# Kernel tuning notes

Measured on AMD Instinct MI355X. Metric: run time of the kernel, lower is better.

The kernel has to match this reference:

```python
import jax, jax.numpy as jnp
import numpy as np

N = 50000      # nodes
E = 800000     # edges (avg degree 16)
D_IN = 128
H = 128
D_OUT = 32


def setup_inputs() -> dict:
    key = jax.random.key(0)
    ks = jax.random.split(key, 12)
    s = 0.05
    return {
        "x": jax.random.normal(ks[0], (N, D_IN), jnp.float32),
        "edge_index": jax.random.randint(ks[1], (2, E), 0, N, jnp.int32),
        "W_in": jax.random.normal(ks[2], (D_IN, H), jnp.float32) * s,
        "b_in": jnp.zeros((H,), jnp.float32),
        "W_msg0": jax.random.normal(ks[3], (H, H), jnp.float32) * s,
        "gru_wih0": jax.random.normal(ks[4], (3 * H, H), jnp.float32) * s,
        "gru_whh0": jax.random.normal(ks[5], (3 * H, H), jnp.float32) * s,
        "gru_bih0": jnp.zeros((3 * H,), jnp.float32),
        "gru_bhh0": jnp.zeros((3 * H,), jnp.float32),
        "W_msg1": jax.random.normal(ks[6], (H, H), jnp.float32) * s,
        "gru_wih1": jax.random.normal(ks[7], (3 * H, H), jnp.float32) * s,
        "gru_whh1": jax.random.normal(ks[8], (3 * H, H), jnp.float32) * s,
        "gru_bih1": jnp.zeros((3 * H,), jnp.float32),
        "gru_bhh1": jnp.zeros((3 * H,), jnp.float32),
        "W_out": jax.random.normal(ks[9], (H, D_OUT), jnp.float32) * s,
        "b_out": jnp.zeros((D_OUT,), jnp.float32),
    }


def _gated_layer(h, src, dst, W_msg, wih, whh, bih, bhh):
    # GatedGraphConv (num_layers=1): linear -> scatter-add over edges -> GRU update
    m = h @ W_msg                                           # [N, H]
    agg = jax.ops.segment_sum(m[src], dst, num_segments=N)  # gather at src, add at dst
    gi = agg @ wih.T + bih                                  # [N, 3H]
    gh = h @ whh.T + bhh                                    # [N, 3H]
    i_r, i_z, i_n = jnp.split(gi, 3, axis=-1)
    h_r, h_z, h_n = jnp.split(gh, 3, axis=-1)
    r = jax.nn.sigmoid(i_r + h_r)
    z = jax.nn.sigmoid(i_z + h_z)
    n = jnp.tanh(i_n + r * h_n)
    return (1.0 - z) * n + z * h


def reference(x, edge_index, W_in, b_in,
              W_msg0, gru_wih0, gru_whh0, gru_bih0, gru_bhh0,
              W_msg1, gru_wih1, gru_whh1, gru_bih1, gru_bhh1,
              W_out, b_out):
    src, dst = edge_index[0], edge_index[1]
    h = jax.nn.relu(x @ W_in + b_in)
    h = _gated_layer(h, src, dst, W_msg0, gru_wih0, gru_whh0, gru_bih0, gru_bhh0)
    h = _gated_layer(h, src, dst, W_msg1, gru_wih1, gru_whh1, gru_bih1, gru_bhh1)
    return h @ W_out + b_out
```

## Files before the change

### kernel.cpp

```cpp
#include <hip/hip_runtime.h>
#include <hip/hip_bf16.h>
#include <math.h>

#define NN 50000
#define NE 800000
#define HD 128
#define SCAN_BLOCKS 196
#define FILL_CHUNK 4096
#define FILL_CHUNKS ((NE + FILL_CHUNK - 1) / FILL_CHUNK)
#define NPART 8

typedef __attribute__((ext_vector_type(8))) short bf16x8;
typedef __attribute__((ext_vector_type(4))) float f32x4;

__device__ inline float b2f(unsigned short s) {
    union { unsigned int u; float f; } w; w.u = ((unsigned int)s) << 16; return w.f;
}
__device__ inline short f2b(float f) {
    __hip_bfloat16 h = __float2bfloat16(f);
    short s; __builtin_memcpy(&s, &h, 2); return s;
}

__global__ void hist_kernel(const int* __restrict__ dst, int* __restrict__ counts) {
    int e = blockIdx.x * blockDim.x + threadIdx.x;
    if (e < NE) atomicAdd(&counts[dst[e]], 1);
}

__global__ __launch_bounds__(256) void scan_partial_kernel(const int* __restrict__ counts,
                                                           int* __restrict__ partial) {
    __shared__ int sm[256];
    int i = blockIdx.x * 256 + threadIdx.x;
    sm[threadIdx.x] = (i < NN) ? counts[i] : 0;
    __syncthreads();
    for (int off = 128; off > 0; off >>= 1) {
        if (threadIdx.x < off) sm[threadIdx.x] += sm[threadIdx.x + off];
        __syncthreads();
    }
    if (threadIdx.x == 0) partial[blockIdx.x] = sm[0];
}

__global__ __launch_bounds__(256) void scan_base_kernel(const int* __restrict__ partial,
                                                        int* __restrict__ base) {
    __shared__ int sm[256];
    int tid = threadIdx.x;
    int v = (tid < SCAN_BLOCKS) ? partial[tid] : 0;
    sm[tid] = v;
    __syncthreads();
    for (int off = 1; off < 256; off <<= 1) {
        int t = (tid >= off) ? sm[tid - off] : 0;
        __syncthreads();
        sm[tid] += t;
        __syncthreads();
    }
    if (tid < SCAN_BLOCKS) base[tid] = sm[tid] - v;
}

__global__ __launch_bounds__(256) void scan_final_kernel(const int* __restrict__ counts,
                                                         const int* __restrict__ base,
                                                         int* __restrict__ offsets,
                                                         int* __restrict__ cursor) {
    __shared__ int sm[256];
    int tid = threadIdx.x;
    int i = blockIdx.x * 256 + tid;
    int v = (i < NN) ? counts[i] : 0;
    sm[tid] = v;
    __syncthreads();
    for (int off = 1; off < 256; off <<= 1) {
        int t = (tid >= off) ? sm[tid - off] : 0;
        __syncthreads();
        sm[tid] += t;
        __syncthreads();
    }
    if (i < NN) {
        int o = base[blockIdx.x] + sm[tid] - v;
        offsets[i] = o;
        cursor[i]  = o;
        if (i == NN - 1) offsets[NN] = o + v;
    }
}

__global__ __launch_bounds__(256) void fill_part_kernel(const int* __restrict__ src,
                                                        const int* __restrict__ dst,
                                                        int* __restrict__ cursor,
                                                        int* __restrict__ perm_src) {
    int part  = blockIdx.x & (NPART - 1);
    int chunk = blockIdx.x >> 3;
    int lo = part * (NN / NPART);
    int hi = (part == NPART - 1) ? NN : lo + (NN / NPART);
    int e0 = chunk * FILL_CHUNK;
    int e1 = min(e0 + FILL_CHUNK, NE);
    for (int e = e0 + threadIdx.x; e < e1; e += 256) {
        int d = dst[e];
        if (d >= lo && d < hi) {
            int pos = atomicAdd(&cursor[d], 1);
            perm_src[pos] = src[e];
        }
    }
}

__global__ void pack_all(const float* W_in, const float* W_msg0, const float* W_msg1,
                         const float* W_out, const float* wih0, const float* whh0,
                         const float* wih1, const float* whh1,
                         short* pWin, short* pWm0, short* pWm1, short* pWout,
                         short* pI0, short* pH0, short* pI1, short* pH1) {
    const float* src; short* dst; int JT; bool kmajor; int J;
    switch (blockIdx.y) {
        case 0: src = W_in;   dst = pWin;  JT = 8;  kmajor = true;  J = 128; break;
        case 1: src = W_msg0; dst = pWm0;  JT = 8;  kmajor = true;  J = 128; break;
        case 2: src = W_msg1; dst = pWm1;  JT = 8;  kmajor = true;  J = 128; break;
        case 3: src = W_out;  dst = pWout; JT = 2;  kmajor = true;  J = 32;  break;
        case 4: src = wih0;   dst = pI0;   JT = 24; kmajor = false; J = 384; break;
        case 5: src = whh0;   dst = pH0;   JT = 24; kmajor = false; J = 384; break;
        case 6: src = wih1;   dst = pI1;   JT = 24; kmajor = false; J = 384; break;
        default: src = whh1;  dst = pH1;   JT = 24; kmajor = false; J = 384; break;
    }
    int t = blockIdx.x * 256 + threadIdx.x;
    if (t >= JT * 4 * 64) return;
    int l = t & 63, ks = (t >> 6) & 3, jt = t >> 8;
    int j = jt * 16 + (l & 15);
    int k0 = ks * 32 + (l >> 4) * 8;
    bf16x8 tv;
    if (kmajor) {
        #pragma unroll
        for (int i = 0; i < 8; ++i) tv[i] = f2b(src[(k0 + i) * J + j]);
    } else {
        #pragma unroll
        for (int i = 0; i < 8; ++i) tv[i] = f2b(src[j * 128 + k0 + i]);
    }
    *reinterpret_cast<bf16x8*>(dst + t * 8) = tv;
}

template<int JT, bool RELU, bool AF32, bool OUTF32>
__global__ __launch_bounds__(256) void gemm_mfma(const void* __restrict__ Av,
                                                 const short* __restrict__ Bp,
                                                 const float* __restrict__ bias,
                                                 void* __restrict__ Cv) {
    int w = threadIdx.x >> 6;
    int l = threadIdx.x & 63;
    int r0 = blockIdx.x * 128 + w * 32;
    int lr = l & 15;
    int lk = (l >> 4) * 8;

    bf16x8 a[2][4];
    #pragma unroll
    for (int mt = 0; mt < 2; ++mt) {
        int row = r0 + mt * 16 + lr;
        if (row > NN - 1) row = NN - 1;
        #pragma unroll
        for (int ks = 0; ks < 4; ++ks) {
            if (AF32) {
                const float* ap = (const float*)Av + (size_t)row * HD + ks * 32 + lk;
                float4 v0 = *(const float4*)ap;
                float4 v1 = *(const float4*)(ap + 4);
                bf16x8 tv;
                tv[0] = f2b(v0.x); tv[1] = f2b(v0.y); tv[2] = f2b(v0.z); tv[3] = f2b(v0.w);
                tv[4] = f2b(v1.x); tv[5] = f2b(v1.y); tv[6] = f2b(v1.z); tv[7] = f2b(v1.w);
                a[mt][ks] = tv;
            } else {
                a[mt][ks] = *reinterpret_cast<const bf16x8*>((const short*)Av + (size_t)row * HD + ks * 32 + lk);
            }
        }
    }

    #pragma unroll
    for (int jt = 0; jt < JT; ++jt) {
        f32x4 acc0 = {0.f, 0.f, 0.f, 0.f}, acc1 = {0.f, 0.f, 0.f, 0.f};
        const short* bp = Bp + ((jt * 4) * 64 + l) * 8;
        #pragma unroll
        for (int ks = 0; ks < 4; ++ks) {
            bf16x8 b = *reinterpret_cast<const bf16x8*>(bp + ks * 64 * 8);
            acc0 = __builtin_amdgcn_mfma_f32_16x16x32_bf16(a[0][ks], b, acc0, 0, 0, 0);
            acc1 = __builtin_amdgcn_mfma_f32_16x16x32_bf16(a[1][ks], b, acc1, 0, 0, 0);
        }
        int col = jt * 16 + lr;
        float bs = bias ? bias[col] : 0.f;
        #pragma unroll
        for (int mt = 0; mt < 2; ++mt) {
            f32x4 acc = mt ? acc1 : acc0;
            #pragma unroll
            for (int rg = 0; rg < 4; ++rg) {
                int row = r0 + mt * 16 + (l >> 4) * 4 + rg;
                if (row < NN) {
                    float v = acc[rg] + bs;
                    if (RELU) v = fmaxf(v, 0.f);
                    if (OUTF32) ((float*)Cv)[(size_t)row * (16 * JT) + col] = v;
                    else        ((short*)Cv)[(size_t)row * (16 * JT) + col] = f2b(v);
                }
            }
        }
    }
}

__global__ __launch_bounds__(256) void aggregate_bf16(const short* __restrict__ m,
                                                      const int* __restrict__ offsets,
                                                      const int* __restrict__ perm_src,
                                                      short* __restrict__ agg) {
    int node = blockIdx.x * 8 + (threadIdx.x >> 5);
    if (node >= NN) return;
    int q = (threadIdx.x & 31) * 4;
    int beg = offsets[node], end = offsets[node + 1];
    float a0 = 0.f, a1 = 0.f, a2 = 0.f, a3 = 0.f;
    int e = beg;
    for (; e + 2 <= end; e += 2) {
        int s0 = perm_src[e], s1 = perm_src[e + 1];
        ushort4 u0 = *reinterpret_cast<const ushort4*>(m + (size_t)s0 * HD + q);
        ushort4 u1 = *reinterpret_cast<const ushort4*>(m + (size_t)s1 * HD + q);
        a0 += b2f(u0.x) + b2f(u1.x);
        a1 += b2f(u0.y) + b2f(u1.y);
        a2 += b2f(u0.z) + b2f(u1.z);
        a3 += b2f(u0.w) + b2f(u1.w);
    }
    if (e < end) {
        ushort4 u = *reinterpret_cast<const ushort4*>(m + (size_t)perm_src[e] * HD + q);
        a0 += b2f(u.x); a1 += b2f(u.y); a2 += b2f(u.z); a3 += b2f(u.w);
    }
    ushort4 o;
    o.x = (unsigned short)f2b(a0); o.y = (unsigned short)f2b(a1);
    o.z = (unsigned short)f2b(a2); o.w = (unsigned short)f2b(a3);
    *reinterpret_cast<ushort4*>(agg + (size_t)node * HD + q) = o;
}

__global__ __launch_bounds__(256) void gru_mfma(const short* __restrict__ agg,
                                                const short* __restrict__ h,
                                                const short* __restrict__ BpI,
                                                const short* __restrict__ BpH,
                                                const float* __restrict__ bih,
                                                const float* __restrict__ bhh,
                                                short* __restrict__ hout) {
    int w = threadIdx.x >> 6;
    int l = threadIdx.x & 63;
    int r0 = blockIdx.x * 64 + w * 16;
    int lr = l & 15;
    int lk = (l >> 4) * 8;

    bf16x8 aa[4], ah[4];
    {
        int row = r0 + lr;
        if (row > NN - 1) row = NN - 1;
        #pragma unroll
        for (int ks = 0; ks < 4; ++ks) {
            aa[ks] = *reinterpret_cast<const bf16x8*>(agg + (size_t)row * HD + ks * 32 + lk);
            ah[ks] = *reinterpret_cast<const bf16x8*>(h   + (size_t)row * HD + ks * 32 + lk);
        }
    }

    const f32x4 zero = {0.f, 0.f, 0.f, 0.f};
    #pragma unroll 1
    for (int jt = 0; jt < 8; ++jt) {
        f32x4 ir = zero, iz = zero, in_ = zero;
        f32x4 hr = zero, hz = zero, hn = zero;
        #pragma unroll
        for (int ks = 0; ks < 4; ++ks) {
            const short* bi = BpI + ((jt * 4 + ks) * 64 + l) * 8;
            const short* bh = BpH + ((jt * 4 + ks) * 64 + l) * 8;
            bf16x8 bir = *reinterpret_cast<const bf16x8*>(bi);
            bf16x8 biz = *reinterpret_cast<const bf16x8*>(bi + 8 * 4 * 64 * 8);
            bf16x8 bin = *reinterpret_cast<const bf16x8*>(bi + 16 * 4 * 64 * 8);
            bf16x8 bhr = *reinterpret_cast<const bf16x8*>(bh);
            bf16x8 bhz = *reinterpret_cast<const bf16x8*>(bh + 8 * 4 * 64 * 8);
            bf16x8 bhn = *reinterpret_cast<const bf16x8*>(bh + 16 * 4 * 64 * 8);
            ir  = __builtin_amdgcn_mfma_f32_16x16x32_bf16(aa[ks], bir, ir,  0, 0, 0);
            iz  = __builtin_amdgcn_mfma_f32_16x16x32_bf16(aa[ks], biz, iz,  0, 0, 0);
            in_ = __builtin_amdgcn_mfma_f32_16x16x32_bf16(aa[ks], bin, in_, 0, 0, 0);
            hr  = __builtin_amdgcn_mfma_f32_16x16x32_bf16(ah[ks], bhr, hr,  0, 0, 0);
            hz  = __builtin_amdgcn_mfma_f32_16x16x32_bf16(ah[ks], bhz, hz,  0, 0, 0);
            hn  = __builtin_amdgcn_mfma_f32_16x16x32_bf16(ah[ks], bhn, hn,  0, 0, 0);
        }
        int col = jt * 16 + lr;
        float bir_ = bih[col], biz_ = bih[128 + col], bin_ = bih[256 + col];
        float bhr_ = bhh[col], bhz_ = bhh[128 + col], bhn_ = bhh[256 + col];
        #pragma unroll
        for (int rg = 0; rg < 4; ++rg) {
            int row = r0 + (l >> 4) * 4 + rg;
            if (row < NN) {
                float rr = 1.f / (1.f + __expf(-(ir[rg] + bir_ + hr[rg] + bhr_)));
                float zz = 1.f / (1.f + __expf(-(iz[rg] + biz_ + hz[rg] + bhz_)));
                float pre = in_[rg] + bin_ + rr * (hn[rg] + bhn_);
                pre = fminf(fmaxf(pre, -20.f), 20.f);
                float e2 = __expf(2.f * pre);
                float nn_ = (e2 - 1.f) / (e2 + 1.f);
                float hv = b2f((unsigned short)h[(size_t)row * HD + col]);
                hout[(size_t)row * HD + col] = f2b((1.f - zz) * nn_ + zz * hv);
            }
        }
    }
}

extern "C" void kernel_launch(void* const* d_in, const int* in_sizes, int n_in,
                              void* d_out, int out_size, void* d_ws, size_t ws_size,
                              hipStream_t stream) {
    const float* x      = (const float*)d_in[0];
    const int*   eidx   = (const int*)d_in[1];
    const float* W_in   = (const float*)d_in[2];
    const float* b_in   = (const float*)d_in[3];
    const float* W_msg0 = (const float*)d_in[4];
    const float* wih0   = (const float*)d_in[5];
    const float* whh0   = (const float*)d_in[6];
    const float* bih0   = (const float*)d_in[7];
    const float* bhh0   = (const float*)d_in[8];
    const float* W_msg1 = (const float*)d_in[9];
    const float* wih1   = (const float*)d_in[10];
    const float* whh1   = (const float*)d_in[11];
    const float* bih1   = (const float*)d_in[12];
    const float* bhh1   = (const float*)d_in[13];
    const float* W_out  = (const float*)d_in[14];
    const float* b_out  = (const float*)d_in[15];
    float* out = (float*)d_out;

    const int* src = eidx;
    const int* dst = eidx + NE;

    char* ws = (char*)d_ws;
    size_t off = 0;
    auto alloc = [&](size_t bytes) {
        void* p = ws + off;
        off += (bytes + 255) & ~(size_t)255;
        return p;
    };
    short* bufA = (short*)alloc((size_t)NN * HD * 2);
    short* bufB = (short*)alloc((size_t)NN * HD * 2);
    short* bufC = (short*)alloc((size_t)NN * HD * 2);
    short* pWin  = (short*)alloc(8  * 4 * 64 * 8 * 2);
    short* pWm0  = (short*)alloc(8  * 4 * 64 * 8 * 2);
    short* pWm1  = (short*)alloc(8  * 4 * 64 * 8 * 2);
    short* pWout = (short*)alloc(2  * 4 * 64 * 8 * 2);
    short* pI0   = (short*)alloc(24 * 4 * 64 * 8 * 2);
    short* pH0   = (short*)alloc(24 * 4 * 64 * 8 * 2);
    short* pI1   = (short*)alloc(24 * 4 * 64 * 8 * 2);
    short* pH1   = (short*)alloc(24 * 4 * 64 * 8 * 2);
    int* counts  = (int*)alloc(NN * 4);
    int* offsets = (int*)alloc((NN + 1) * 4);
    int* cursor  = (int*)alloc(NN * 4);
    int* perm    = (int*)alloc(NE * 4);
    int* partial = (int*)alloc(SCAN_BLOCKS * 4);
    int* pbase   = (int*)alloc(SCAN_BLOCKS * 4);

    hipMemsetAsync(counts, 0, NN * 4, stream);
    hist_kernel<<<(NE + 255) / 256, 256, 0, stream>>>(dst, counts);
    scan_partial_kernel<<<SCAN_BLOCKS, 256, 0, stream>>>(counts, partial);
    scan_base_kernel<<<1, 256, 0, stream>>>(partial, pbase);
    scan_final_kernel<<<SCAN_BLOCKS, 256, 0, stream>>>(counts, pbase, offsets, cursor);
    fill_part_kernel<<<NPART * FILL_CHUNKS, 256, 0, stream>>>(src, dst, cursor, perm);

    pack_all<<<dim3(24, 8), 256, 0, stream>>>(W_in, W_msg0, W_msg1, W_out,
                                              wih0, whh0, wih1, whh1,
                                              pWin, pWm0, pWm1, pWout, pI0, pH0, pI1, pH1);

    int g   = (NN + 127) / 128;
    int g64 = (NN + 63) / 64;

    gemm_mfma<8, true, true, false><<<g, 256, 0, stream>>>(x, pWin, b_in, bufA);

    gemm_mfma<8, false, false, false><<<g, 256, 0, stream>>>(bufA, pWm0, nullptr, bufB);
    aggregate_bf16<<<(NN + 7) / 8, 256, 0, stream>>>(bufB, offsets, perm, bufC);
    gru_mfma<<<g64, 256, 0, stream>>>(bufC, bufA, pI0, pH0, bih0, bhh0, bufB);

    gemm_mfma<8, false, false, false><<<g, 256, 0, stream>>>(bufB, pWm1, nullptr, bufA);
    aggregate_bf16<<<(NN + 7) / 8, 256, 0, stream>>>(bufA, offsets, perm, bufC);
    gru_mfma<<<g64, 256, 0, stream>>>(bufC, bufB, pI1, pH1, bih1, bhh1, bufA);

    gemm_mfma<2, false, false, true><<<g, 256, 0, stream>>>(bufA, pWout, b_out, out);
}
```

Baseline: 387.7 us.

## Fuse chained GEMMs through LDS and merge histogram with weight packing

Fuses the input projection with the first message GEMM, and each GRU update with the following message or output GEMM. The intermediate hidden tile is staged in XOR-swizzled LDS per wave instead of being written to and re-read from global memory. The histogram and weight-packing kernels are merged into one launch. This removes several kernel launches and some global round trips. In exchange, the fused kernels use a smaller 64-row tile, add LDS use and a barrier, and the last layer no longer writes its hidden state.

```diff
diff --git a/kernel.cpp b/kernel.cpp
--- a/kernel.cpp
+++ b/kernel.cpp
@@ -9,6 +9,7 @@
 #define FILL_CHUNK 4096
 #define FILL_CHUNKS ((NE + FILL_CHUNK - 1) / FILL_CHUNK)
 #define NPART 8
+#define HIST_BLOCKS ((NE + 255) / 256)
 
 typedef __attribute__((ext_vector_type(8))) short bf16x8;
 typedef __attribute__((ext_vector_type(4))) float f32x4;
@@ -21,9 +22,45 @@
     short s; __builtin_memcpy(&s, &h, 2); return s;
 }
 
-__global__ void hist_kernel(const int* __restrict__ dst, int* __restrict__ counts) {
-    int e = blockIdx.x * blockDim.x + threadIdx.x;
-    if (e < NE) atomicAdd(&counts[dst[e]], 1);
+__global__ void prep_kernel(const int* __restrict__ dst, int* __restrict__ counts,
+                            const float* W_in, const float* W_msg0, const float* W_msg1,
+                            const float* W_out, const float* wih0, const float* whh0,
+                            const float* wih1, const float* whh1,
+                            short* pWin, short* pWm0, short* pWm1, short* pWout,
+                            short* pI0, short* pH0, short* pI1, short* pH1) {
+    int b = blockIdx.x;
+    if (b < HIST_BLOCKS) {
+        int e = b * 256 + threadIdx.x;
+        if (e < NE) atomicAdd(&counts[dst[e]], 1);
+        return;
+    }
+    int pb = b - HIST_BLOCKS;
+    int px = pb % 24, wsel = pb / 24;
+    const float* src; short* dstp; int JT; bool kmajor; int J;
+    switch (wsel) {
+        case 0: src = W_in;   dstp = pWin;  JT = 8;  kmajor = true;  J = 128; break;
+        case 1: src = W_msg0; dstp = pWm0;  JT = 8;  kmajor = true;  J = 128; break;
+        case 2: src = W_msg1; dstp = pWm1;  JT = 8;  kmajor = true;  J = 128; break;
+        case 3: src = W_out;  dstp = pWout; JT = 2;  kmajor = true;  J = 32;  break;
+        case 4: src = wih0;   dstp = pI0;   JT = 24; kmajor = false; J = 384; break;
+        case 5: src = whh0;   dstp = pH0;   JT = 24; kmajor = false; J = 384; break;
+        case 6: src = wih1;   dstp = pI1;   JT = 24; kmajor = false; J = 384; break;
+        default: src = whh1;  dstp = pH1;   JT = 24; kmajor = false; J = 384; break;
+    }
+    int t = px * 256 + threadIdx.x;
+    if (t >= JT * 4 * 64) return;
+    int l = t & 63, ks = (t >> 6) & 3, jt = t >> 8;
+    int j = jt * 16 + (l & 15);
+    int k0 = ks * 32 + (l >> 4) * 8;
+    bf16x8 tv;
+    if (kmajor) {
+        #pragma unroll
+        for (int i = 0; i < 8; ++i) tv[i] = f2b(src[(k0 + i) * J + j]);
+    } else {
+        #pragma unroll
+        for (int i = 0; i < 8; ++i) tv[i] = f2b(src[j * 128 + k0 + i]);
+    }
+    *reinterpret_cast<bf16x8*>(dstp + t * 8) = tv;
 }
 
 __global__ __launch_bounds__(256) void scan_partial_kernel(const int* __restrict__ counts,
@@ -94,99 +131,6 @@
         if (d >= lo && d < hi) {
             int pos = atomicAdd(&cursor[d], 1);
             perm_src[pos] = src[e];
-        }
-    }
-}
-
-__global__ void pack_all(const float* W_in, const float* W_msg0, const float* W_msg1,
-                         const float* W_out, const float* wih0, const float* whh0,
-                         const float* wih1, const float* whh1,
-                         short* pWin, short* pWm0, short* pWm1, short* pWout,
-                         short* pI0, short* pH0, short* pI1, short* pH1) {
-    const float* src; short* dst; int JT; bool kmajor; int J;
-    switch (blockIdx.y) {
-        case 0: src = W_in;   dst = pWin;  JT = 8;  kmajor = true;  J = 128; break;
-        case 1: src = W_msg0; dst = pWm0;  JT = 8;  kmajor = true;  J = 128; break;
-        case 2: src = W_msg1; dst = pWm1;  JT = 8;  kmajor = true;  J = 128; break;
-        case 3: src = W_out;  dst = pWout; JT = 2;  kmajor = true;  J = 32;  break;
-        case 4: src = wih0;   dst = pI0;   JT = 24; kmajor = false; J = 384; break;
-        case 5: src = whh0;   dst = pH0;   JT = 24; kmajor = false; J = 384; break;
-        case 6: src = wih1;   dst = pI1;   JT = 24; kmajor = false; J = 384; break;
-        default: src = whh1;  dst = pH1;   JT = 24; kmajor = false; J = 384; break;
-    }
-    int t = blockIdx.x * 256 + threadIdx.x;
-    if (t >= JT * 4 * 64) return;
-    int l = t & 63, ks = (t >> 6) & 3, jt = t >> 8;
-    int j = jt * 16 + (l & 15);
-    int k0 = ks * 32 + (l >> 4) * 8;
-    bf16x8 tv;
-    if (kmajor) {
-        #pragma unroll
-        for (int i = 0; i < 8; ++i) tv[i] = f2b(src[(k0 + i) * J + j]);
-    } else {
-        #pragma unroll
-        for (int i = 0; i < 8; ++i) tv[i] = f2b(src[j * 128 + k0 + i]);
-    }
-    *reinterpret_cast<bf16x8*>(dst + t * 8) = tv;
-}
-
-template<int JT, bool RELU, bool AF32, bool OUTF32>
-__global__ __launch_bounds__(256) void gemm_mfma(const void* __restrict__ Av,
-                                                 const short* __restrict__ Bp,
-                                                 const float* __restrict__ bias,
-                                                 void* __restrict__ Cv) {
-    int w = threadIdx.x >> 6;
-    int l = threadIdx.x & 63;
-    int r0 = blockIdx.x * 128 + w * 32;
-    int lr = l & 15;
-    int lk = (l >> 4) * 8;
-
-    bf16x8 a[2][4];
-    #pragma unroll
-    for (int mt = 0; mt < 2; ++mt) {
-        int row = r0 + mt * 16 + lr;
-        if (row > NN - 1) row = NN - 1;
-        #pragma unroll
-        for (int ks = 0; ks < 4; ++ks) {
-            if (AF32) {
-                const float* ap = (const float*)Av + (size_t)row * HD + ks * 32 + lk;
-                float4 v0 = *(const float4*)ap;
-                float4 v1 = *(const float4*)(ap + 4);
-                bf16x8 tv;
-                tv[0] = f2b(v0.x); tv[1] = f2b(v0.y); tv[2] = f2b(v0.z); tv[3] = f2b(v0.w);
-                tv[4] = f2b(v1.x); tv[5] = f2b(v1.y); tv[6] = f2b(v1.z); tv[7] = f2b(v1.w);
-                a[mt][ks] = tv;
-            } else {
-                a[mt][ks] = *reinterpret_cast<const bf16x8*>((const short*)Av + (size_t)row * HD + ks * 32 + lk);
-            }
-        }
-    }
-
-    #pragma unroll
-    for (int jt = 0; jt < JT; ++jt) {
-        f32x4 acc0 = {0.f, 0.f, 0.f, 0.f}, acc1 = {0.f, 0.f, 0.f, 0.f};
-        const short* bp = Bp + ((jt * 4) * 64 + l) * 8;
-        #pragma unroll
-        for (int ks = 0; ks < 4; ++ks) {
-            bf16x8 b = *reinterpret_cast<const bf16x8*>(bp + ks * 64 * 8);
-            acc0 = __builtin_amdgcn_mfma_f32_16x16x32_bf16(a[0][ks], b, acc0, 0, 0, 0);
-            acc1 = __builtin_amdgcn_mfma_f32_16x16x32_bf16(a[1][ks], b, acc1, 0, 0, 0);
-        }
-        int col = jt * 16 + lr;
-        float bs = bias ? bias[col] : 0.f;
-        #pragma unroll
-        for (int mt = 0; mt < 2; ++mt) {
-            f32x4 acc = mt ? acc1 : acc0;
-            #pragma unroll
-            for (int rg = 0; rg < 4; ++rg) {
-                int row = r0 + mt * 16 + (l >> 4) * 4 + rg;
-                if (row < NN) {
-                    float v = acc[rg] + bs;
-                    if (RELU) v = fmaxf(v, 0.f);
-                    if (OUTF32) ((float*)Cv)[(size_t)row * (16 * JT) + col] = v;
-                    else        ((short*)Cv)[(size_t)row * (16 * JT) + col] = f2b(v);
-                }
-            }
         }
     }
 }
@@ -220,23 +164,116 @@
     *reinterpret_cast<ushort4*>(agg + (size_t)node * HD + q) = o;
 }
 
-__global__ __launch_bounds__(256) void gru_mfma(const short* __restrict__ agg,
-                                                const short* __restrict__ h,
-                                                const short* __restrict__ BpI,
-                                                const short* __restrict__ BpH,
-                                                const float* __restrict__ bih,
-                                                const float* __restrict__ bhh,
-                                                short* __restrict__ hout) {
-    int w = threadIdx.x >> 6;
-    int l = threadIdx.x & 63;
+template<int JT2, bool OUTF32_2>
+__device__ inline void second_gemm(const short* hw, int l, int r0,
+                                   const short* __restrict__ Bp2,
+                                   const float* __restrict__ bias2,
+                                   void* __restrict__ Cv2) {
+    int lr = l & 15;
+    bf16x8 a2[4];
+    #pragma unroll
+    for (int ks = 0; ks < 4; ++ks) {
+        int row = l & 15;
+        int col = (ks * 32 + (l >> 4) * 8) ^ ((row & 7) << 3);
+        a2[ks] = *reinterpret_cast<const bf16x8*>(hw + row * 128 + col);
+    }
+    const f32x4 zero = {0.f, 0.f, 0.f, 0.f};
+    #pragma unroll
+    for (int jt = 0; jt < JT2; ++jt) {
+        f32x4 acc = zero;
+        const short* bp = Bp2 + ((jt * 4) * 64 + l) * 8;
+        #pragma unroll
+        for (int ks = 0; ks < 4; ++ks) {
+            bf16x8 b = *reinterpret_cast<const bf16x8*>(bp + ks * 64 * 8);
+            acc = __builtin_amdgcn_mfma_f32_16x16x32_bf16(a2[ks], b, acc, 0, 0, 0);
+        }
+        int col = jt * 16 + lr;
+        float bs = bias2 ? bias2[col] : 0.f;
+        #pragma unroll
+        for (int rg = 0; rg < 4; ++rg) {
+            int row = r0 + (l >> 4) * 4 + rg;
+            if (row < NN) {
+                float v = acc[rg] + bs;
+                if (OUTF32_2) ((float*)Cv2)[(size_t)row * (16 * JT2) + col] = v;
+                else          ((short*)Cv2)[(size_t)row * (16 * JT2) + col] = f2b(v);
+            }
+        }
+    }
+}
+
+__global__ __launch_bounds__(256) void fused_in_msg(const float* __restrict__ x,
+                                                    const short* __restrict__ Bp1,
+                                                    const float* __restrict__ bias1,
+                                                    const short* __restrict__ Bp2,
+                                                    short* __restrict__ Hout,
+                                                    short* __restrict__ Mout) {
+    __shared__ short hl[4][2048];
+    int w = threadIdx.x >> 6, l = threadIdx.x & 63;
     int r0 = blockIdx.x * 64 + w * 16;
-    int lr = l & 15;
-    int lk = (l >> 4) * 8;
+    int lr = l & 15, lk = (l >> 4) * 8;
+    short* hw = hl[w];
+
+    bf16x8 a[4];
+    {
+        int row = min(r0 + lr, NN - 1);
+        #pragma unroll
+        for (int ks = 0; ks < 4; ++ks) {
+            const float* ap = x + (size_t)row * HD + ks * 32 + lk;
+            float4 v0 = *(const float4*)ap;
+            float4 v1 = *(const float4*)(ap + 4);
+            bf16x8 tv;
+            tv[0] = f2b(v0.x); tv[1] = f2b(v0.y); tv[2] = f2b(v0.z); tv[3] = f2b(v0.w);
+            tv[4] = f2b(v1.x); tv[5] = f2b(v1.y); tv[6] = f2b(v1.z); tv[7] = f2b(v1.w);
+            a[ks] = tv;
+        }
+    }
+
+    const f32x4 zero = {0.f, 0.f, 0.f, 0.f};
+    #pragma unroll
+    for (int jt = 0; jt < 8; ++jt) {
+        f32x4 acc = zero;
+        const short* bp = Bp1 + ((jt * 4) * 64 + l) * 8;
+        #pragma unroll
+        for (int ks = 0; ks < 4; ++ks) {
+            bf16x8 b = *reinterpret_cast<const bf16x8*>(bp + ks * 64 * 8);
+            acc = __builtin_amdgcn_mfma_f32_16x16x32_bf16(a[ks], b, acc, 0, 0, 0);
+        }
+        int col = jt * 16 + lr;
+        float bs = bias1[col];
+        #pragma unroll
+        for (int rg = 0; rg < 4; ++rg) {
+            int row16 = (l >> 4) * 4 + rg;
+            int grow = r0 + row16;
+            float v = fmaxf(acc[rg] + bs, 0.f);
+            short hb = f2b(v);
+            hw[row16 * 128 + (col ^ ((row16 & 7) << 3))] = hb;
+            if (grow < NN) Hout[(size_t)grow * HD + col] = hb;
+        }
+    }
+    __syncthreads();
+    second_gemm<8, false>(hw, l, r0, Bp2, nullptr, Mout);
+}
+
+template<int JT2, bool OUTF32_2, bool WRITE_H>
+__global__ __launch_bounds__(256) void fused_gru(const short* __restrict__ agg,
+                                                 const short* __restrict__ h,
+                                                 const short* __restrict__ BpI,
+                                                 const short* __restrict__ BpH,
+                                                 const float* __restrict__ bih,
+                                                 const float* __restrict__ bhh,
+                                                 const short* __restrict__ Bp2,
+                                                 const float* __restrict__ bias2,
+                                                 short* __restrict__ Hout,
+                                                 void* __restrict__ Cv2) {
+    __shared__ short hl[4][2048];
+    int w = threadIdx.x >> 6, l = threadIdx.x & 63;
+    int r0 = blockIdx.x * 64 + w * 16;
+    int lr = l & 15, lk = (l >> 4) * 8;
+    short* hw = hl[w];
 
     bf16x8 aa[4], ah[4];
     {
-        int row = r0 + lr;
-        if (row > NN - 1) row = NN - 1;
+        int row = min(r0 + lr, NN - 1);
         #pragma unroll
         for (int ks = 0; ks < 4; ++ks) {
             aa[ks] = *reinterpret_cast<const bf16x8*>(agg + (size_t)row * HD + ks * 32 + lk);
@@ -271,19 +308,24 @@
         float bhr_ = bhh[col], bhz_ = bhh[128 + col], bhn_ = bhh[256 + col];
         #pragma unroll
         for (int rg = 0; rg < 4; ++rg) {
-            int row = r0 + (l >> 4) * 4 + rg;
-            if (row < NN) {
-                float rr = 1.f / (1.f + __expf(-(ir[rg] + bir_ + hr[rg] + bhr_)));
-                float zz = 1.f / (1.f + __expf(-(iz[rg] + biz_ + hz[rg] + bhz_)));
-                float pre = in_[rg] + bin_ + rr * (hn[rg] + bhn_);
-                pre = fminf(fmaxf(pre, -20.f), 20.f);
-                float e2 = __expf(2.f * pre);
-                float nn_ = (e2 - 1.f) / (e2 + 1.f);
-                float hv = b2f((unsigned short)h[(size_t)row * HD + col]);
-                hout[(size_t)row * HD + col] = f2b((1.f - zz) * nn_ + zz * hv);
-            }
-        }
-    }
+            int row16 = (l >> 4) * 4 + rg;
+            int grow = r0 + row16;
+            int crow = min(grow, NN - 1);
+            float rr = 1.f / (1.f + __expf(-(ir[rg] + bir_ + hr[rg] + bhr_)));
+            float zz = 1.f / (1.f + __expf(-(iz[rg] + biz_ + hz[rg] + bhz_)));
+            float pre = in_[rg] + bin_ + rr * (hn[rg] + bhn_);
+            pre = fminf(fmaxf(pre, -20.f), 20.f);
+            float e2 = __expf(2.f * pre);
+            float nn_ = (e2 - 1.f) / (e2 + 1.f);
+            float hv = b2f((unsigned short)h[(size_t)crow * HD + col]);
+            float nh = (1.f - zz) * nn_ + zz * hv;
+            short hb = f2b(nh);
+            hw[row16 * 128 + (col ^ ((row16 & 7) << 3))] = hb;
+            if (WRITE_H && grow < NN) Hout[(size_t)grow * HD + col] = hb;
+        }
+    }
+    __syncthreads();
+    second_gemm<JT2, OUTF32_2>(hw, l, r0, Bp2, bias2, Cv2);
 }
 
 extern "C" void kernel_launch(void* const* d_in, const int* in_sizes, int n_in,
@@ -336,28 +378,23 @@
     int* pbase   = (int*)alloc(SCAN_BLOCKS * 4);
 
     hipMemsetAsync(counts, 0, NN * 4, stream);
-    hist_kernel<<<(NE + 255) / 256, 256, 0, stream>>>(dst, counts);
+    prep_kernel<<<HIST_BLOCKS + 192, 256, 0, stream>>>(dst, counts,
+        W_in, W_msg0, W_msg1, W_out, wih0, whh0, wih1, whh1,
+        pWin, pWm0, pWm1, pWout, pI0, pH0, pI1, pH1);
     scan_partial_kernel<<<SCAN_BLOCKS, 256, 0, stream>>>(counts, partial);
     scan_base_kernel<<<1, 256, 0, stream>>>(partial, pbase);
     scan_final_kernel<<<SCAN_BLOCKS, 256, 0, stream>>>(counts, pbase, offsets, cursor);
     fill_part_kernel<<<NPART * FILL_CHUNKS, 256, 0, stream>>>(src, dst, cursor, perm);
 
-    pack_all<<<dim3(24, 8), 256, 0, stream>>>(W_in, W_msg0, W_msg1, W_out,
-                                              wih0, whh0, wih1, whh1,
-                                              pWin, pWm0, pWm1, pWout, pI0, pH0, pI1, pH1);
-
-    int g   = (NN + 127) / 128;
     int g64 = (NN + 63) / 64;
 
-    gemm_mfma<8, true, true, false><<<g, 256, 0, stream>>>(x, pWin, b_in, bufA);
-
-    gemm_mfma<8, false, false, false><<<g, 256, 0, stream>>>(bufA, pWm0, nullptr, bufB);
+    fused_in_msg<<<g64, 256, 0, stream>>>(x, pWin, b_in, pWm0, bufA, bufB);
+
     aggregate_bf16<<<(NN + 7) / 8, 256, 0, stream>>>(bufB, offsets, perm, bufC);
-    gru_mfma<<<g64, 256, 0, stream>>>(bufC, bufA, pI0, pH0, bih0, bhh0, bufB);
-
-    gemm_mfma<8, false, false, false><<<g, 256, 0, stream>>>(bufB, pWm1, nullptr, bufA);
+    fused_gru<8, false, true><<<g64, 256, 0, stream>>>(bufC, bufA, pI0, pH0, bih0, bhh0,
+                                                       pWm1, nullptr, bufB, bufA);
+
     aggregate_bf16<<<(NN + 7) / 8, 256, 0, stream>>>(bufA, offsets, perm, bufC);
-    gru_mfma<<<g64, 256, 0, stream>>>(bufC, bufB, pI1, pH1, bih1, bhh1, bufA);
-
-    gemm_mfma<2, false, false, true><<<g, 256, 0, stream>>>(bufA, pWout, b_out, out);
-}
+    fused_gru<2, true, false><<<g64, 256, 0, stream>>>(bufC, bufB, pI1, pH1, bih1, bhh1,
+                                                       pWout, b_out, nullptr, out);
+}
```

After: 360.2 us. 1.08x faster.
